# Kernel tuning notes

Hardware: AMD Instinct MI355X
Metric: run time of the kernel (lower is better)

The kernel has to match this reference:

```python
import jax, jax.numpy as jnp
import numpy as np

B, S, QD = 4, 2048, 1024
NH, KVH, DH = 16, 4, 64
WIN = 256  # sliding_window


def setup_inputs() -> dict:
    key = jax.random.key(0)
    ks = jax.random.split(key, 5)
    s = QD ** -0.5
    return {
        "hidden_states": jax.random.normal(ks[0], (B, S, QD), jnp.float32),
        "Wq": jax.random.normal(ks[1], (QD, NH * DH), jnp.float32) * s,
        "Wk": jax.random.normal(ks[2], (QD, KVH * DH), jnp.float32) * s,
        "Wv": jax.random.normal(ks[3], (QD, KVH * DH), jnp.float32) * s,
        "Wo": jax.random.normal(ks[4], (NH * DH, QD), jnp.float32) * s,
    }


def reference(hidden_states, Wq, Wk, Wv, Wo):
    x = hidden_states
    # QKV projections (torch Linear, no bias)
    q = (x @ Wq).reshape(B, S, NH, DH).transpose(0, 2, 1, 3)    # [B,NH,S,DH]
    k = (x @ Wk).reshape(B, S, KVH, DH).transpose(0, 2, 1, 3)   # [B,KVH,S,DH]
    v = (x @ Wv).reshape(B, S, KVH, DH).transpose(0, 2, 1, 3)
    # GQA: instead of repeat_interleave on k/v, group query heads per kv head
    g = NH // KVH
    qg = q.reshape(B, KVH, g, S, DH)
    scale = DH ** -0.5
    scores = jnp.einsum('bkgsd,bktd->bkgst', qg, k) * scale      # [B,KVH,g,S,S]
    # Sliding-window mask: torch SDPA treats a FLOAT mask as ADDITIVE, and the
    # original builds a 0/1 float mask (1 where |i-j| <= window). Faithful: add it.
    idx = jnp.arange(S)
    win = (jnp.abs(idx[:, None] - idx[None, :]) <= WIN).astype(scores.dtype)  # [S,S]
    scores = scores + win  # broadcast over B,KVH,g (same mask for all batch/heads)
    attn = jax.nn.softmax(scores, axis=-1)
    out = jnp.einsum('bkgst,bktd->bkgsd', attn, v)               # [B,KVH,g,S,DH]
    out = out.reshape(B, NH, S, DH).transpose(0, 2, 1, 3).reshape(B, S, NH * DH)
    return out @ Wo
```

## Files before the change

kernel.cpp:

```cpp
#include <hip/hip_runtime.h>
#include <hip/hip_bf16.h>


using short8 = __attribute__((ext_vector_type(8))) short;
using f32x2  = __attribute__((ext_vector_type(2))) float;
using f32x4  = __attribute__((ext_vector_type(4))) float;
using f32x16 = __attribute__((ext_vector_type(16))) float;
using uint2v = __attribute__((ext_vector_type(2))) unsigned int;

#define GLDS(g, l) __builtin_amdgcn_global_load_lds( \
    (const __attribute__((address_space(1))) void*)(g), \
    (__attribute__((address_space(3))) void*)(l), 16, 0, 0)

__device__ __forceinline__ unsigned short f2bf(float f) {
  union { float f; unsigned u; } v; v.f = f;
  unsigned r = v.u + 0x7fffu + ((v.u >> 16) & 1u);
  return (unsigned short)(r >> 16);
}

__device__ __forceinline__ unsigned cvtpk(float lo, float hi) {
  unsigned r;
  asm("v_cvt_pk_bf16_f32 %0, %1, %2" : "=v"(r) : "v"(lo), "v"(hi));
  return r;
}

__device__ __forceinline__ f32x2 mk2(float a, float b) { f32x2 r; r[0] = a; r[1] = b; return r; }

__device__ __forceinline__ f32x2 pk_add(f32x2 a, f32x2 b) {
  f32x2 r;
  asm("v_pk_add_f32 %0, %1, %2" : "=v"(r) : "v"(a), "v"(b));
  return r;
}

__device__ __forceinline__ f32x2 pk_fma(f32x2 a, f32x2 b, f32x2 c) {
  f32x2 r;
  asm("v_pk_fma_f32 %0, %1, %2, %3" : "=v"(r) : "v"(a), "v"(b), "v"(c));
  return r;
}

__global__ __launch_bounds__(256) void wtr_kernel(
    const float* __restrict__ Wq, const float* __restrict__ Wk,
    const float* __restrict__ Wv, const float* __restrict__ Wo,
    unsigned short* __restrict__ WqkvT, unsigned short* __restrict__ WoT)
{
  __shared__ float tile[32][33];
  const int bx = blockIdx.x;
  const int by = blockIdx.y;
  const float* src; unsigned short* dst; int C, ct;
  if (by < 32)      { src = Wq; dst = WqkvT;               C = 1024; ct = by; }
  else if (by < 40) { src = Wk; dst = WqkvT + 1024 * 1024; C = 256;  ct = by - 32; }
  else if (by < 48) { src = Wv; dst = WqkvT + 1280 * 1024; C = 256;  ct = by - 40; }
  else              { src = Wo; dst = WoT;                 C = 1024; ct = by - 48; }
  const int tx = threadIdx.x & 31, ty = threadIdx.x >> 5;
  const int c0 = ct * 32, r0 = bx * 32;
#pragma unroll
  for (int i = 0; i < 4; ++i)
    tile[ty + i * 8][tx] = src[(size_t)(r0 + ty + i * 8) * C + c0 + tx];
  __syncthreads();
#pragma unroll
  for (int i = 0; i < 4; ++i) {
    int c = ty + i * 8;
    dst[(size_t)(c0 + c) * 1024 + r0 + tx] = f2bf(tile[tx][c]);
  }
}

__global__ __launch_bounds__(256) void qkv_gemm_kernel(
    const float* __restrict__ X, const unsigned short* __restrict__ Bt,
    unsigned short* __restrict__ Qo, unsigned short* __restrict__ Ko,
    unsigned short* __restrict__ Vto)
{
  __shared__ __align__(16) unsigned short As[128 * 32];
  __shared__ __align__(16) unsigned short Bs[128 * 32];
  const int m0 = blockIdx.x * 128;
  const int n0 = blockIdx.y * 128;
  const int t = threadIdx.x;
  const int w = t >> 6, l = t & 63;
  const int wr = w >> 1, wc = w & 1;

  f32x4 acc[4][4] = {};

  const size_t aoff = (size_t)(m0 + w * 16 + (l >> 2)) * 1024 + (size_t)((l & 3) * 8);
  const size_t boff = (size_t)(n0 + w * 16 + (l >> 2)) * 1024 + (size_t)((l & 3) * 8);
  unsigned short* Aw0 = &As[w * 512 + l * 8];
  unsigned short* Aw1 = &As[(w + 4) * 512 + l * 8];
  const bool qk = (n0 < 1280);

  for (int kt = 0; kt < 1024; kt += 32) {
    GLDS(Bt + boff + kt,             &Bs[w * 512]);
    GLDS(Bt + boff + 64 * 1024 + kt, &Bs[(w + 4) * 512]);
    float4 fa0 = *reinterpret_cast<const float4*>(X + aoff + kt);
    float4 fa1 = *reinterpret_cast<const float4*>(X + aoff + kt + 4);
    float4 fb0 = *reinterpret_cast<const float4*>(X + aoff + 64 * 1024 + kt);
    float4 fb1 = *reinterpret_cast<const float4*>(X + aoff + 64 * 1024 + kt + 4);
    uint4 ua, ub;
    ua.x = cvtpk(fa0.x, fa0.y); ua.y = cvtpk(fa0.z, fa0.w);
    ua.z = cvtpk(fa1.x, fa1.y); ua.w = cvtpk(fa1.z, fa1.w);
    ub.x = cvtpk(fb0.x, fb0.y); ub.y = cvtpk(fb0.z, fb0.w);
    ub.z = cvtpk(fb1.x, fb1.y); ub.w = cvtpk(fb1.z, fb1.w);
    *reinterpret_cast<uint4*>(Aw0) = ua;
    *reinterpret_cast<uint4*>(Aw1) = ub;
    __syncthreads();

    short8 af[4], bfr[4];
#pragma unroll
    for (int mi = 0; mi < 4; ++mi) {
      int row = wr * 64 + mi * 16 + (l & 15);
      af[mi] = *reinterpret_cast<const short8*>(&As[row * 32 + (l >> 4) * 8]);
    }
#pragma unroll
    for (int ni = 0; ni < 4; ++ni) {
      int row = wc * 64 + ni * 16 + (l & 15);
      bfr[ni] = *reinterpret_cast<const short8*>(&Bs[row * 32 + (l >> 4) * 8]);
    }
    if (qk) {
#pragma unroll
      for (int mi = 0; mi < 4; ++mi)
#pragma unroll
        for (int ni = 0; ni < 4; ++ni)
          acc[mi][ni] = __builtin_amdgcn_mfma_f32_16x16x32_bf16(bfr[ni], af[mi], acc[mi][ni], 0, 0, 0);
    } else {
#pragma unroll
      for (int mi = 0; mi < 4; ++mi)
#pragma unroll
        for (int ni = 0; ni < 4; ++ni)
          acc[mi][ni] = __builtin_amdgcn_mfma_f32_16x16x32_bf16(af[mi], bfr[ni], acc[mi][ni], 0, 0, 0);
    }
    __syncthreads();
  }

  const int lo = (l >> 4) * 4;

  if (qk) {
#pragma unroll
    for (int mi = 0; mi < 4; ++mi) {
      const int tok = m0 + wr * 64 + mi * 16 + (l & 15);
      const int bb = tok >> 11, ss = tok & 2047;
      const int T5 = ss >> 5, q5 = ss & 31;
#pragma unroll
      for (int ni = 0; ni < 4; ++ni) {
        const int ddb = n0 + wc * 64 + ni * 16;
        uint2 wv;
        wv.x = cvtpk(acc[mi][ni][0], acc[mi][ni][1]);
        wv.y = cvtpk(acc[mi][ni][2], acc[mi][ni][3]);
        size_t base; unsigned short* dstp;
        if (ddb < 1024) {
          int hh = ddb >> 6, kk = (ddb >> 4) & 3;
          base = ((((size_t)(bb * 16 + hh)) * 64 + T5) * 4 + kk) * 512; dstp = Qo;
        } else {
          int kvh = (ddb - 1024) >> 6, kk = (ddb >> 4) & 3;
          base = ((((size_t)(bb * 4 + kvh)) * 64 + T5) * 4 + kk) * 512; dstp = Ko;
        }
        *reinterpret_cast<uint2*>(dstp + base + (lo >> 3) * 256 + q5 * 8 + (lo & 7)) = wv;
      }
    }
  } else {
#pragma unroll
    for (int ni = 0; ni < 4; ++ni) {
      const int dd = n0 + wc * 64 + ni * 16 + (l & 15);
      const int kvh = (dd - 1280) >> 6, d6 = dd & 63;
#pragma unroll
      for (int mi = 0; mi < 4; ++mi) {
        const int tokb = m0 + wr * 64 + mi * 16 + lo;
        const int bb = tokb >> 11, ss = tokb & 2047;
        const int T5 = ss >> 5;
        const int f = (d6 >> 5) * 2 + (mi & 1);
        uint2 wv;
        wv.x = cvtpk(acc[mi][ni][0], acc[mi][ni][1]);
        wv.y = cvtpk(acc[mi][ni][2], acc[mi][ni][3]);
        size_t base = ((((size_t)(bb * 4 + kvh)) * 64 + T5) * 4 + f) * 512;
        *reinterpret_cast<uint2*>(Vto + base + ((lo >> 3) & 1) * 256 + (d6 & 31) * 8 + (lo & 7)) = wv;
      }
    }
  }
}

__global__ __launch_bounds__(256) void outproj_gemm_kernel(
    const unsigned short* __restrict__ A, const unsigned short* __restrict__ Bt,
    float* __restrict__ Co)
{
  __shared__ __align__(16) unsigned short As[128 * 32];
  __shared__ __align__(16) unsigned short Bs[128 * 32];
  const int m0 = blockIdx.x * 128;
  const int n0 = blockIdx.y * 128;
  const int t = threadIdx.x;
  const int w = t >> 6, l = t & 63;
  const int wr = w >> 1, wc = w & 1;

  f32x4 acc[4][4] = {};

  const size_t aoff = (size_t)(m0 + w * 16 + (l >> 2)) * 1024 + (size_t)((l & 3) * 8);
  const size_t boff = (size_t)(n0 + w * 16 + (l >> 2)) * 1024 + (size_t)((l & 3) * 8);

  for (int kt = 0; kt < 1024; kt += 32) {
    GLDS(A  + aoff + kt,             &As[w * 512]);
    GLDS(A  + aoff + 64 * 1024 + kt, &As[(w + 4) * 512]);
    GLDS(Bt + boff + kt,             &Bs[w * 512]);
    GLDS(Bt + boff + 64 * 1024 + kt, &Bs[(w + 4) * 512]);
    __syncthreads();

    short8 af[4], bfr[4];
#pragma unroll
    for (int mi = 0; mi < 4; ++mi) {
      int row = wr * 64 + mi * 16 + (l & 15);
      af[mi] = *reinterpret_cast<const short8*>(&As[row * 32 + (l >> 4) * 8]);
    }
#pragma unroll
    for (int ni = 0; ni < 4; ++ni) {
      int row = wc * 64 + ni * 16 + (l & 15);
      bfr[ni] = *reinterpret_cast<const short8*>(&Bs[row * 32 + (l >> 4) * 8]);
    }
#pragma unroll
    for (int mi = 0; mi < 4; ++mi)
#pragma unroll
      for (int ni = 0; ni < 4; ++ni)
        acc[mi][ni] = __builtin_amdgcn_mfma_f32_16x16x32_bf16(af[mi], bfr[ni], acc[mi][ni], 0, 0, 0);
    __syncthreads();
  }

#pragma unroll
  for (int mi = 0; mi < 4; ++mi)
#pragma unroll
    for (int ni = 0; ni < 4; ++ni)
#pragma unroll
      for (int r = 0; r < 4; ++r) {
        int m = m0 + wr * 64 + mi * 16 + (l >> 4) * 4 + r;
        int n = n0 + wc * 64 + ni * 16 + (l & 15);
        Co[((size_t)m << 10) + n] = acc[mi][ni][r];
      }
}

__global__ __launch_bounds__(256, 4) void attn_kernel(
    const unsigned short* __restrict__ Qf, const unsigned short* __restrict__ Kf,
    const unsigned short* __restrict__ Vf, unsigned short* __restrict__ AO)
{
  const int t = threadIdx.x, w = t >> 6, l = t & 63;
  const int hi = l >> 5, ln = l & 31;

  const int orig = blockIdx.x;
  const int swz = (orig & 7) * 128 + (orig >> 3);
  const int hf = swz >> 4;
  const int qt = swz & 15;
  const int b = hf >> 4, h = hf & 15, kvh = h >> 2;
  const int q0 = qt * 128 + w * 32;
  const int qrow = q0 + ln;

  const unsigned short* Qp = Qf + (((size_t)hf * 64 + qt * 4 + w) * 4) * 512;
  const unsigned short* Kt = Kf + ((size_t)(b * 4 + kvh) * 256) * 512 + l * 8;
  const unsigned short* Vt = Vf + ((size_t)(b * 4 + kvh) * 256) * 512 + l * 8;

  short8 qf[4];
#pragma unroll
  for (int kk = 0; kk < 4; ++kk)
    qf[kk] = *reinterpret_cast<const short8*>(Qp + kk * 512 + l * 8);

  f32x16 oA = {}, oB = {};
  float lsum = 0.f;
  const float C1  = 0.125f * 1.44269504f;
  const float L2E = 1.44269504f;
  const float FM  = 12.0f;
  const f32x2 C1p = mk2(C1, C1);

  for (int T = 0; T < 64; ++T) {
    short8 kf0 = *reinterpret_cast<const short8*>(Kt);
    short8 kf1 = *reinterpret_cast<const short8*>(Kt + 512);
    short8 kf2 = *reinterpret_cast<const short8*>(Kt + 1024);
    short8 kf3 = *reinterpret_cast<const short8*>(Kt + 1536);
    f32x16 s = {};
    s = __builtin_amdgcn_mfma_f32_32x32x16_bf16(kf0, qf[0], s, 0, 0, 0);
    s = __builtin_amdgcn_mfma_f32_32x32x16_bf16(kf1, qf[1], s, 0, 0, 0);
    s = __builtin_amdgcn_mfma_f32_32x32x16_bf16(kf2, qf[2], s, 0, 0, 0);
    s = __builtin_amdgcn_mfma_f32_32x32x16_bf16(kf3, qf[3], s, 0, 0, 0);
    short8 vf0 = *reinterpret_cast<const short8*>(Vt);
    short8 vf1 = *reinterpret_cast<const short8*>(Vt + 512);
    short8 vf2 = *reinterpret_cast<const short8*>(Vt + 1024);
    short8 vf3 = *reinterpret_cast<const short8*>(Vt + 1536);
    Kt += 2048; Vt += 2048;

    const int kv0 = T * 32;
    const int d = q0 - kv0;
    float p[16];
    if (d == 256 || d == -256) {
      const int qmb = qrow - kv0 - 4 * hi;
#pragma unroll
      for (int r = 0; r < 16; ++r) {
        const int kc = (r & 3) + 8 * (r >> 2);
        int df = qmb - kc; df = df < 0 ? -df : df;
        p[r] = __builtin_amdgcn_exp2f(
            __builtin_fmaf(s[r], C1, (df <= 256 ? L2E : 0.f) - FM));
      }
    } else {
      const float cc = ((d <= 224 && d >= -224) ? L2E : 0.f) - FM;
      const f32x2 ccp = mk2(cc, cc);
#pragma unroll
      for (int j = 0; j < 8; ++j) {
        f32x2 sv = mk2(s[2 * j], s[2 * j + 1]);
        f32x2 tv = pk_fma(sv, C1p, ccp);
        p[2 * j]     = __builtin_amdgcn_exp2f(tv[0]);
        p[2 * j + 1] = __builtin_amdgcn_exp2f(tv[1]);
      }
    }

    {
      f32x2 a0v = mk2(p[0], p[1]),  a1v = mk2(p[8],  p[9]);
      f32x2 b0v = mk2(p[2], p[3]),  b1v = mk2(p[10], p[11]);
      f32x2 c0v = mk2(p[4], p[5]),  c1v = mk2(p[12], p[13]);
      f32x2 d0v = mk2(p[6], p[7]),  d1v = mk2(p[14], p[15]);
      f32x2 q0v = pk_add(a0v, a1v);
      f32x2 q1v = pk_add(b0v, b1v);
      f32x2 q2v = pk_add(c0v, c1v);
      f32x2 q3v = pk_add(d0v, d1v);
      f32x2 r0 = pk_add(q0v, q2v);
      f32x2 r1 = pk_add(q1v, q3v);
      f32x2 u  = pk_add(r0, r1);
      float sum = u[0] + u[1];
      uint2v sw = __builtin_amdgcn_permlane32_swap(__float_as_uint(sum), __float_as_uint(sum), false, false);
      lsum += __uint_as_float(sw[0]) + __uint_as_float(sw[1]);
    }

#pragma unroll
    for (int ks = 0; ks < 2; ++ks) {
      unsigned a0 = cvtpk(p[ks * 8 + 0], p[ks * 8 + 1]);
      unsigned a1 = cvtpk(p[ks * 8 + 2], p[ks * 8 + 3]);
      unsigned b0 = cvtpk(p[ks * 8 + 4], p[ks * 8 + 5]);
      unsigned b1 = cvtpk(p[ks * 8 + 6], p[ks * 8 + 7]);
      uint2v s0 = __builtin_amdgcn_permlane32_swap(a0, b0, false, false);
      uint2v s1 = __builtin_amdgcn_permlane32_swap(a1, b1, false, false);
      union { unsigned u[4]; short8 v; } pf;
      pf.u[0] = s0[0]; pf.u[1] = s1[0]; pf.u[2] = s0[1]; pf.u[3] = s1[1];
      oA = __builtin_amdgcn_mfma_f32_32x32x16_bf16(ks ? vf1 : vf0, pf.v, oA, 0, 0, 0);
      oB = __builtin_amdgcn_mfma_f32_32x32x16_bf16(ks ? vf3 : vf2, pf.v, oB, 0, 0, 0);
    }
  }

  const float inv = 1.f / lsum;
  unsigned short* Op = AO + ((size_t)(b * 2048 + qrow)) * 1024 + h * 64;
#pragma unroll
  for (int qd = 0; qd < 4; ++qd) {
    uint2 wv;
    wv.x = cvtpk(oA[4 * qd + 0] * inv, oA[4 * qd + 1] * inv);
    wv.y = cvtpk(oA[4 * qd + 2] * inv, oA[4 * qd + 3] * inv);
    *reinterpret_cast<uint2*>(Op + qd * 8 + hi * 4) = wv;
  }
#pragma unroll
  for (int qd = 0; qd < 4; ++qd) {
    uint2 wv;
    wv.x = cvtpk(oB[4 * qd + 0] * inv, oB[4 * qd + 1] * inv);
    wv.y = cvtpk(oB[4 * qd + 2] * inv, oB[4 * qd + 3] * inv);
    *reinterpret_cast<uint2*>(Op + 32 + qd * 8 + hi * 4) = wv;
  }
}

extern "C" void kernel_launch(void* const* d_in, const int* in_sizes, int n_in,
                              void* d_out, int out_size, void* d_ws, size_t ws_size,
                              hipStream_t stream)
{
  const float* X  = (const float*)d_in[0];
  const float* Wq = (const float*)d_in[1];
  const float* Wk = (const float*)d_in[2];
  const float* Wv = (const float*)d_in[3];
  const float* Wo = (const float*)d_in[4];
  float* out = (float*)d_out;
  char* ws = (char*)d_ws;

  unsigned short* WqkvT = (unsigned short*)(ws);
  unsigned short* WoT   = (unsigned short*)(ws + 3145728);
  unsigned short* Q     = (unsigned short*)(ws + 5242880);
  unsigned short* Kc    = (unsigned short*)(ws + 22020096);
  unsigned short* Vt    = (unsigned short*)(ws + 26214400);
  unsigned short* AO    = (unsigned short*)(ws + 30408704);

  wtr_kernel<<<dim3(32, 80), 256, 0, stream>>>(Wq, Wk, Wv, Wo, WqkvT, WoT);
  qkv_gemm_kernel<<<dim3(64, 12), 256, 0, stream>>>(X, WqkvT, Q, Kc, Vt);
  attn_kernel<<<1024, 256, 0, stream>>>(Q, Kc, Vt, AO);
  outproj_gemm_kernel<<<dim3(64, 8), 256, 0, stream>>>(AO, WoT, out);
}
```

Measured before the change: 197.6 us.

## Double K-step per barrier in GEMMs, swizzle block order, add MFMA priority hints

Result: faster. 191.4 us, median of 2 (-3.1%).

```diff
diff --git a/kernel.cpp b/kernel.cpp
--- a/kernel.cpp
+++ b/kernel.cpp
@@ -69,10 +69,12 @@
     unsigned short* __restrict__ Qo, unsigned short* __restrict__ Ko,
     unsigned short* __restrict__ Vto)
 {
-  __shared__ __align__(16) unsigned short As[128 * 32];
-  __shared__ __align__(16) unsigned short Bs[128 * 32];
-  const int m0 = blockIdx.x * 128;
-  const int n0 = blockIdx.y * 128;
+  __shared__ __align__(16) unsigned short As[2 * 4096];
+  __shared__ __align__(16) unsigned short Bs[2 * 4096];
+  const int id = blockIdx.x;
+  const int swz = (id & 7) * 96 + (id >> 3);
+  const int m0 = (swz & 63) * 128;
+  const int n0 = (swz >> 6) * 128;
   const int t = threadIdx.x;
   const int w = t >> 6, l = t & 63;
   const int wr = w >> 1, wc = w & 1;
@@ -81,49 +83,53 @@
 
   const size_t aoff = (size_t)(m0 + w * 16 + (l >> 2)) * 1024 + (size_t)((l & 3) * 8);
   const size_t boff = (size_t)(n0 + w * 16 + (l >> 2)) * 1024 + (size_t)((l & 3) * 8);
-  unsigned short* Aw0 = &As[w * 512 + l * 8];
-  unsigned short* Aw1 = &As[(w + 4) * 512 + l * 8];
   const bool qk = (n0 < 1280);
 
-  for (int kt = 0; kt < 1024; kt += 32) {
-    GLDS(Bt + boff + kt,             &Bs[w * 512]);
-    GLDS(Bt + boff + 64 * 1024 + kt, &Bs[(w + 4) * 512]);
-    float4 fa0 = *reinterpret_cast<const float4*>(X + aoff + kt);
-    float4 fa1 = *reinterpret_cast<const float4*>(X + aoff + kt + 4);
-    float4 fb0 = *reinterpret_cast<const float4*>(X + aoff + 64 * 1024 + kt);
-    float4 fb1 = *reinterpret_cast<const float4*>(X + aoff + 64 * 1024 + kt + 4);
-    uint4 ua, ub;
-    ua.x = cvtpk(fa0.x, fa0.y); ua.y = cvtpk(fa0.z, fa0.w);
-    ua.z = cvtpk(fa1.x, fa1.y); ua.w = cvtpk(fa1.z, fa1.w);
-    ub.x = cvtpk(fb0.x, fb0.y); ub.y = cvtpk(fb0.z, fb0.w);
-    ub.z = cvtpk(fb1.x, fb1.y); ub.w = cvtpk(fb1.z, fb1.w);
-    *reinterpret_cast<uint4*>(Aw0) = ua;
-    *reinterpret_cast<uint4*>(Aw1) = ub;
+  for (int kt = 0; kt < 1024; kt += 64) {
+#pragma unroll
+    for (int p = 0; p < 2; ++p) {
+      GLDS(Bt + boff + kt + p * 32,             &Bs[p * 4096 + w * 512]);
+      GLDS(Bt + boff + 64 * 1024 + kt + p * 32, &Bs[p * 4096 + (w + 4) * 512]);
+      float4 fa0 = *reinterpret_cast<const float4*>(X + aoff + kt + p * 32);
+      float4 fa1 = *reinterpret_cast<const float4*>(X + aoff + kt + p * 32 + 4);
+      float4 fb0 = *reinterpret_cast<const float4*>(X + aoff + 64 * 1024 + kt + p * 32);
+      float4 fb1 = *reinterpret_cast<const float4*>(X + aoff + 64 * 1024 + kt + p * 32 + 4);
+      uint4 ua, ub;
+      ua.x = cvtpk(fa0.x, fa0.y); ua.y = cvtpk(fa0.z, fa0.w);
+      ua.z = cvtpk(fa1.x, fa1.y); ua.w = cvtpk(fa1.z, fa1.w);
+      ub.x = cvtpk(fb0.x, fb0.y); ub.y = cvtpk(fb0.z, fb0.w);
+      ub.z = cvtpk(fb1.x, fb1.y); ub.w = cvtpk(fb1.z, fb1.w);
+      *reinterpret_cast<uint4*>(&As[p * 4096 + w * 512 + l * 8]) = ua;
+      *reinterpret_cast<uint4*>(&As[p * 4096 + (w + 4) * 512 + l * 8]) = ub;
+    }
     __syncthreads();
 
-    short8 af[4], bfr[4];
-#pragma unroll
-    for (int mi = 0; mi < 4; ++mi) {
-      int row = wr * 64 + mi * 16 + (l & 15);
-      af[mi] = *reinterpret_cast<const short8*>(&As[row * 32 + (l >> 4) * 8]);
-    }
-#pragma unroll
-    for (int ni = 0; ni < 4; ++ni) {
-      int row = wc * 64 + ni * 16 + (l & 15);
-      bfr[ni] = *reinterpret_cast<const short8*>(&Bs[row * 32 + (l >> 4) * 8]);
-    }
-    if (qk) {
-#pragma unroll
-      for (int mi = 0; mi < 4; ++mi)
-#pragma unroll
-        for (int ni = 0; ni < 4; ++ni)
-          acc[mi][ni] = __builtin_amdgcn_mfma_f32_16x16x32_bf16(bfr[ni], af[mi], acc[mi][ni], 0, 0, 0);
-    } else {
-#pragma unroll
-      for (int mi = 0; mi < 4; ++mi)
-#pragma unroll
-        for (int ni = 0; ni < 4; ++ni)
-          acc[mi][ni] = __builtin_amdgcn_mfma_f32_16x16x32_bf16(af[mi], bfr[ni], acc[mi][ni], 0, 0, 0);
+#pragma unroll
+    for (int p = 0; p < 2; ++p) {
+      short8 af[4], bfr[4];
+#pragma unroll
+      for (int mi = 0; mi < 4; ++mi) {
+        int row = wr * 64 + mi * 16 + (l & 15);
+        af[mi] = *reinterpret_cast<const short8*>(&As[p * 4096 + row * 32 + (l >> 4) * 8]);
+      }
+#pragma unroll
+      for (int ni = 0; ni < 4; ++ni) {
+        int row = wc * 64 + ni * 16 + (l & 15);
+        bfr[ni] = *reinterpret_cast<const short8*>(&Bs[p * 4096 + row * 32 + (l >> 4) * 8]);
+      }
+      if (qk) {
+#pragma unroll
+        for (int mi = 0; mi < 4; ++mi)
+#pragma unroll
+          for (int ni = 0; ni < 4; ++ni)
+            acc[mi][ni] = __builtin_amdgcn_mfma_f32_16x16x32_bf16(bfr[ni], af[mi], acc[mi][ni], 0, 0, 0);
+      } else {
+#pragma unroll
+        for (int mi = 0; mi < 4; ++mi)
+#pragma unroll
+          for (int ni = 0; ni < 4; ++ni)
+            acc[mi][ni] = __builtin_amdgcn_mfma_f32_16x16x32_bf16(af[mi], bfr[ni], acc[mi][ni], 0, 0, 0);
+      }
     }
     __syncthreads();
   }
@@ -178,10 +184,12 @@
     const unsigned short* __restrict__ A, const unsigned short* __restrict__ Bt,
     float* __restrict__ Co)
 {
-  __shared__ __align__(16) unsigned short As[128 * 32];
-  __shared__ __align__(16) unsigned short Bs[128 * 32];
-  const int m0 = blockIdx.x * 128;
-  const int n0 = blockIdx.y * 128;
+  __shared__ __align__(16) unsigned short As[2 * 4096];
+  __shared__ __align__(16) unsigned short Bs[2 * 4096];
+  const int id = blockIdx.x;
+  const int swz = (id & 7) * 64 + (id >> 3);
+  const int m0 = (swz & 63) * 128;
+  const int n0 = (swz >> 6) * 128;
   const int t = threadIdx.x;
   const int w = t >> 6, l = t & 63;
   const int wr = w >> 1, wc = w & 1;
@@ -191,29 +199,35 @@
   const size_t aoff = (size_t)(m0 + w * 16 + (l >> 2)) * 1024 + (size_t)((l & 3) * 8);
   const size_t boff = (size_t)(n0 + w * 16 + (l >> 2)) * 1024 + (size_t)((l & 3) * 8);
 
-  for (int kt = 0; kt < 1024; kt += 32) {
-    GLDS(A  + aoff + kt,             &As[w * 512]);
-    GLDS(A  + aoff + 64 * 1024 + kt, &As[(w + 4) * 512]);
-    GLDS(Bt + boff + kt,             &Bs[w * 512]);
-    GLDS(Bt + boff + 64 * 1024 + kt, &Bs[(w + 4) * 512]);
+  for (int kt = 0; kt < 1024; kt += 64) {
+#pragma unroll
+    for (int p = 0; p < 2; ++p) {
+      GLDS(A  + aoff + kt + p * 32,             &As[p * 4096 + w * 512]);
+      GLDS(A  + aoff + 64 * 1024 + kt + p * 32, &As[p * 4096 + (w + 4) * 512]);
+      GLDS(Bt + boff + kt + p * 32,             &Bs[p * 4096 + w * 512]);
+      GLDS(Bt + boff + 64 * 1024 + kt + p * 32, &Bs[p * 4096 + (w + 4) * 512]);
+    }
     __syncthreads();
 
-    short8 af[4], bfr[4];
-#pragma unroll
-    for (int mi = 0; mi < 4; ++mi) {
-      int row = wr * 64 + mi * 16 + (l & 15);
-      af[mi] = *reinterpret_cast<const short8*>(&As[row * 32 + (l >> 4) * 8]);
-    }
-#pragma unroll
-    for (int ni = 0; ni < 4; ++ni) {
-      int row = wc * 64 + ni * 16 + (l & 15);
-      bfr[ni] = *reinterpret_cast<const short8*>(&Bs[row * 32 + (l >> 4) * 8]);
-    }
-#pragma unroll
-    for (int mi = 0; mi < 4; ++mi)
-#pragma unroll
-      for (int ni = 0; ni < 4; ++ni)
-        acc[mi][ni] = __builtin_amdgcn_mfma_f32_16x16x32_bf16(af[mi], bfr[ni], acc[mi][ni], 0, 0, 0);
+#pragma unroll
+    for (int p = 0; p < 2; ++p) {
+      short8 af[4], bfr[4];
+#pragma unroll
+      for (int mi = 0; mi < 4; ++mi) {
+        int row = wr * 64 + mi * 16 + (l & 15);
+        af[mi] = *reinterpret_cast<const short8*>(&As[p * 4096 + row * 32 + (l >> 4) * 8]);
+      }
+#pragma unroll
+      for (int ni = 0; ni < 4; ++ni) {
+        int row = wc * 64 + ni * 16 + (l & 15);
+        bfr[ni] = *reinterpret_cast<const short8*>(&Bs[p * 4096 + row * 32 + (l >> 4) * 8]);
+      }
+#pragma unroll
+      for (int mi = 0; mi < 4; ++mi)
+#pragma unroll
+        for (int ni = 0; ni < 4; ++ni)
+          acc[mi][ni] = __builtin_amdgcn_mfma_f32_16x16x32_bf16(af[mi], bfr[ni], acc[mi][ni], 0, 0, 0);
+    }
     __syncthreads();
   }
 
@@ -265,11 +279,13 @@
     short8 kf1 = *reinterpret_cast<const short8*>(Kt + 512);
     short8 kf2 = *reinterpret_cast<const short8*>(Kt + 1024);
     short8 kf3 = *reinterpret_cast<const short8*>(Kt + 1536);
+    __builtin_amdgcn_s_setprio(1);
     f32x16 s = {};
     s = __builtin_amdgcn_mfma_f32_32x32x16_bf16(kf0, qf[0], s, 0, 0, 0);
     s = __builtin_amdgcn_mfma_f32_32x32x16_bf16(kf1, qf[1], s, 0, 0, 0);
     s = __builtin_amdgcn_mfma_f32_32x32x16_bf16(kf2, qf[2], s, 0, 0, 0);
     s = __builtin_amdgcn_mfma_f32_32x32x16_bf16(kf3, qf[3], s, 0, 0, 0);
+    __builtin_amdgcn_s_setprio(0);
     short8 vf0 = *reinterpret_cast<const short8*>(Vt);
     short8 vf1 = *reinterpret_cast<const short8*>(Vt + 512);
     short8 vf2 = *reinterpret_cast<const short8*>(Vt + 1024);
@@ -327,8 +343,10 @@
       uint2v s1 = __builtin_amdgcn_permlane32_swap(a1, b1, false, false);
       union { unsigned u[4]; short8 v; } pf;
       pf.u[0] = s0[0]; pf.u[1] = s1[0]; pf.u[2] = s0[1]; pf.u[3] = s1[1];
+      __builtin_amdgcn_s_setprio(1);
       oA = __builtin_amdgcn_mfma_f32_32x32x16_bf16(ks ? vf1 : vf0, pf.v, oA, 0, 0, 0);
       oB = __builtin_amdgcn_mfma_f32_32x32x16_bf16(ks ? vf3 : vf2, pf.v, oB, 0, 0, 0);
+      __builtin_amdgcn_s_setprio(0);
     }
   }
 
@@ -370,7 +388,7 @@
   unsigned short* AO    = (unsigned short*)(ws + 30408704);
 
   wtr_kernel<<<dim3(32, 80), 256, 0, stream>>>(Wq, Wk, Wv, Wo, WqkvT, WoT);
-  qkv_gemm_kernel<<<dim3(64, 12), 256, 0, stream>>>(X, WqkvT, Q, Kc, Vt);
+  qkv_gemm_kernel<<<768, 256, 0, stream>>>(X, WqkvT, Q, Kc, Vt);
   attn_kernel<<<1024, 256, 0, stream>>>(Q, Kc, Vt, AO);
-  outproj_gemm_kernel<<<dim3(64, 8), 256, 0, stream>>>(AO, WoT, out);
-}
+  outproj_gemm_kernel<<<512, 256, 0, stream>>>(AO, WoT, out);
+}
```
